# Kernel optimization log

Hardware: AMD Instinct MI355X
Metric: run time of the kernel (lower is better)

The kernel has to match this reference:

```python
import jax, jax.numpy as jnp
import numpy as np

LAMBD = 0.1  # lambd from __init__

N_POINTS = 262144
D_EMBED = 512
N_CLUSTERS = 64


def setup_inputs() -> dict:
    key = jax.random.key(0)
    k1, k2 = jax.random.split(key)
    x = jax.random.normal(k1, (N_POINTS, D_EMBED), dtype=jnp.float32)
    # original init: uniform(-1, 1)
    centroids = jax.random.uniform(k2, (N_CLUSTERS, D_EMBED), dtype=jnp.float32, minval=-1.0, maxval=1.0)
    return {"x": x, "centroids": centroids, "alpha": 100}


def reference(x, centroids, alpha):
    # stack_dist[i, n] = sum_d (x[n,d] - centroids[i,d])^2, fused via the
    x2 = jnp.sum(x * x, axis=1)                      # [N]
    c2 = jnp.sum(centroids * centroids, axis=1)      # [k]
    cross = jnp.einsum('nd,kd->kn', x, centroids)    # [k, N]
    dist = x2[None, :] + c2[:, None] - 2.0 * cross   # [k, N]
    # exp(-alpha*(dist - min)) / sum == softmax(-alpha*dist) along the k axis
    soft = jax.nn.softmax(-jnp.float32(alpha) * dist, axis=0)  # [k, N]
    k_means_loss = LAMBD * jnp.mean(jnp.sum(dist * soft, axis=0))
    return k_means_loss
```

## Files before the change

### kernel.cpp

```cpp
#include <hip/hip_runtime.h>
#include <hip/hip_bf16.h>

#define N_POINTS   262144
#define D_EMBED    512
#define N_CLUSTERS 64
#define LAMBD      0.1f

#define BLK_PTS 64
#define KC      128
#define NCHUNK  (D_EMBED / KC)
#define ROWP    (KC + 8)

typedef __attribute__((ext_vector_type(8))) short  short8;
typedef __attribute__((ext_vector_type(4))) float  f32x4;

__device__ __forceinline__ unsigned short f2bf(float f) {
    union { float f; unsigned u; } v; v.f = f;
    unsigned u = v.u;
    return (unsigned short)((u + 0x7FFFu + ((u >> 16) & 1u)) >> 16);
}

__global__ void prep_kernel(const float* __restrict__ cent,
                            float* __restrict__ c2_ws,
                            unsigned short* __restrict__ afrag_ws,
                            float* __restrict__ out) {
    const int k    = blockIdx.x;
    const int lane = threadIdx.x;
    const float* row = cent + (size_t)k * D_EMBED;

    float4 v0 = ((const float4*)row)[lane * 2 + 0];
    float4 v1 = ((const float4*)row)[lane * 2 + 1];

    float s = v0.x*v0.x + v0.y*v0.y + v0.z*v0.z + v0.w*v0.w
            + v1.x*v1.x + v1.y*v1.y + v1.z*v1.z + v1.w*v1.w;
    #pragma unroll
    for (int m = 1; m < 64; m <<= 1) s += __shfl_xor(s, m);
    if (lane == 0) c2_ws[k] = s;

    const int sstep = lane >> 2;
    const int q     = lane & 3;
    const int t     = k >> 4;
    const size_t idx8 = ((size_t)(sstep * 4 + t) * 64 + q * 16 + (k & 15)) * 8;

    ushort4 h0, h1;
    h0.x = f2bf(v0.x); h0.y = f2bf(v0.y); h0.z = f2bf(v0.z); h0.w = f2bf(v0.w);
    h1.x = f2bf(v1.x); h1.y = f2bf(v1.y); h1.z = f2bf(v1.z); h1.w = f2bf(v1.w);
    *(ushort4*)&afrag_ws[idx8 + 0] = h0;
    *(ushort4*)&afrag_ws[idx8 + 4] = h1;

    if (k == 0 && lane == 0) *out = 0.0f;
}

__global__ __launch_bounds__(256, 4)
void main_kernel(const float* __restrict__ x,
                 const int* __restrict__ alpha_p,
                 const float* __restrict__ c2_ws,
                 const unsigned short* __restrict__ afrag_ws,
                 float* __restrict__ out) {
    __shared__ unsigned short xlds[BLK_PTS * ROWP];
    __shared__ float c2s[N_CLUSTERS];
    __shared__ float x2s[BLK_PTS];
    __shared__ float blocksum_s[4];

    const int tid  = threadIdx.x;
    const int lane = tid & 63;
    const int w    = tid >> 6;
    const size_t base = (size_t)blockIdx.x * BLK_PTS;

    if (tid < 64) { c2s[tid] = c2_ws[tid]; x2s[tid] = 0.0f; }
    __syncthreads();

    const float alpha = (float)alpha_p[0];
    const int p = lane & 15;
    const int q = lane >> 4;

    f32x4 acc[4] = {f32x4{0,0,0,0}, f32x4{0,0,0,0}, f32x4{0,0,0,0}, f32x4{0,0,0,0}};

    for (int c = 0; c < NCHUNK; ++c) {
        #pragma unroll
        for (int it = 0; it < 8; ++it) {
            const int f    = it * 256 + tid;
            const int row  = f >> 5;
            const int col4 = f & 31;
            float4 v = ((const float4*)(x + (base + row) * D_EMBED + c * KC))[col4];

            float sq = v.x*v.x + v.y*v.y + v.z*v.z + v.w*v.w;
            sq += __shfl_xor(sq, 1);
            sq += __shfl_xor(sq, 2);
            sq += __shfl_xor(sq, 4);
            sq += __shfl_xor(sq, 8);
            sq += __shfl_xor(sq, 16);
            if ((lane & 31) == 0) x2s[row] += sq;

            ushort4 h;
            h.x = f2bf(v.x); h.y = f2bf(v.y); h.z = f2bf(v.z); h.w = f2bf(v.w);
            *(ushort4*)&xlds[row * ROWP + col4 * 4] = h;
        }
        __syncthreads();

        #pragma unroll
        for (int sl = 0; sl < 4; ++sl) {
            const int s = c * 4 + sl;
            short8 b = *(const short8*)&xlds[(16 * w + p) * ROWP + sl * 32 + q * 8];
            #pragma unroll
            for (int t = 0; t < 4; ++t) {
                short8 a = *(const short8*)&afrag_ws[((size_t)(s * 4 + t) * 64 + lane) * 8];
                acc[t] = __builtin_amdgcn_mfma_f32_16x16x32_bf16(a, b, acc[t], 0, 0, 0);
            }
        }
        __syncthreads();
    }

    const float x2 = x2s[16 * w + p];
    float dist[16];
    float minv = 1e30f;
    #pragma unroll
    for (int t = 0; t < 4; ++t) {
        #pragma unroll
        for (int r = 0; r < 4; ++r) {
            const int cl = 16 * t + q * 4 + r;
            const float d = x2 + c2s[cl] - 2.0f * acc[t][r];
            dist[t * 4 + r] = d;
            minv = fminf(minv, d);
        }
    }
    minv = fminf(minv, __shfl_xor(minv, 16));
    minv = fminf(minv, __shfl_xor(minv, 32));

    float esum = 0.0f, wsum = 0.0f;
    #pragma unroll
    for (int i = 0; i < 16; ++i) {
        const float e = __expf(-alpha * (dist[i] - minv));
        esum += e;
        wsum += dist[i] * e;
    }
    esum += __shfl_xor(esum, 16);
    esum += __shfl_xor(esum, 32);
    wsum += __shfl_xor(wsum, 16);
    wsum += __shfl_xor(wsum, 32);

    float pv = wsum / esum;
    #pragma unroll
    for (int m = 1; m < 64; m <<= 1) pv += __shfl_xor(pv, m);

    if (lane == 0) blocksum_s[w] = pv;
    __syncthreads();
    if (tid == 0) {
        const float T = blocksum_s[0] + blocksum_s[1] + blocksum_s[2] + blocksum_s[3];
        atomicAdd(out, T * (LAMBD / (4.0f * (float)N_POINTS)));
    }
}

extern "C" void kernel_launch(void* const* d_in, const int* in_sizes, int n_in,
                              void* d_out, int out_size, void* d_ws, size_t ws_size,
                              hipStream_t stream) {
    const float* x      = (const float*)d_in[0];
    const float* cent   = (const float*)d_in[1];
    const int*   alphap = (const int*)d_in[2];
    float* out = (float*)d_out;

    float*          c2_ws = (float*)d_ws;
    unsigned short* afrag = (unsigned short*)((char*)d_ws + 256);

    hipLaunchKernelGGL(prep_kernel, dim3(N_CLUSTERS), dim3(64), 0, stream,
                       cent, c2_ws, afrag, out);
    hipLaunchKernelGGL(main_kernel, dim3(N_POINTS / BLK_PTS), dim3(256), 0, stream,
                       x, alphap, c2_ws, afrag, out);
}
```

Measured before the change: 714.3 us.

## Load x directly into 32x32x16 MFMA operands, dropping LDS staging

Each wave now handles 32 points and loads its x rows straight from global memory into registers, converting them to bf16 operands for 32x32x16 MFMA. This removes the LDS tile, the syncthreads, and the per-row shuffle reductions of the squared norm. Each lane sums the squared norm for its own slice of the row, and one shuffle finishes it. The centroid fragments are re-laid out in the prep kernel to match the new MFMA operand shape. In exchange, the per-lane global loads are strided by row (each lane reads 32 bytes per step from a different row), which may hurt coalescing.

```diff
diff --git a/kernel.cpp b/kernel.cpp
--- a/kernel.cpp
+++ b/kernel.cpp
@@ -6,13 +6,11 @@
 #define N_CLUSTERS 64
 #define LAMBD      0.1f
 
-#define BLK_PTS 64
-#define KC      128
-#define NCHUNK  (D_EMBED / KC)
-#define ROWP    (KC + 8)
+#define PTS_PER_WAVE  32
+#define PTS_PER_BLK   128
 
-typedef __attribute__((ext_vector_type(8))) short  short8;
-typedef __attribute__((ext_vector_type(4))) float  f32x4;
+typedef __attribute__((ext_vector_type(8)))  short short8;
+typedef __attribute__((ext_vector_type(16))) float f32x16;
 
 __device__ __forceinline__ unsigned short f2bf(float f) {
     union { float f; unsigned u; } v; v.f = f;
@@ -22,7 +20,7 @@
 
 __global__ void prep_kernel(const float* __restrict__ cent,
                             float* __restrict__ c2_ws,
-                            unsigned short* __restrict__ afrag_ws,
+                            unsigned short* __restrict__ afrag,
                             float* __restrict__ out) {
     const int k    = blockIdx.x;
     const int lane = threadIdx.x;
@@ -37,16 +35,17 @@
     for (int m = 1; m < 64; m <<= 1) s += __shfl_xor(s, m);
     if (lane == 0) c2_ws[k] = s;
 
-    const int sstep = lane >> 2;
-    const int q     = lane & 3;
-    const int t     = k >> 4;
-    const size_t idx8 = ((size_t)(sstep * 4 + t) * 64 + q * 16 + (k & 15)) * 8;
+    const int st = lane >> 1;
+    const int h  = lane & 1;
+    const int t  = k >> 5;
+    const int m  = k & 31;
+    const size_t idx8 = ((size_t)(st * 2 + t) * 64 + m + 32 * h) * 8;
 
     ushort4 h0, h1;
     h0.x = f2bf(v0.x); h0.y = f2bf(v0.y); h0.z = f2bf(v0.z); h0.w = f2bf(v0.w);
     h1.x = f2bf(v1.x); h1.y = f2bf(v1.y); h1.z = f2bf(v1.z); h1.w = f2bf(v1.w);
-    *(ushort4*)&afrag_ws[idx8 + 0] = h0;
-    *(ushort4*)&afrag_ws[idx8 + 4] = h1;
+    *(ushort4*)&afrag[idx8 + 0] = h0;
+    *(ushort4*)&afrag[idx8 + 4] = h1;
 
     if (k == 0 && lane == 0) *out = 0.0f;
 }
@@ -55,99 +54,82 @@
 void main_kernel(const float* __restrict__ x,
                  const int* __restrict__ alpha_p,
                  const float* __restrict__ c2_ws,
-                 const unsigned short* __restrict__ afrag_ws,
+                 const unsigned short* __restrict__ afrag,
                  float* __restrict__ out) {
-    __shared__ unsigned short xlds[BLK_PTS * ROWP];
     __shared__ float c2s[N_CLUSTERS];
-    __shared__ float x2s[BLK_PTS];
-    __shared__ float blocksum_s[4];
+    __shared__ float bsum[4];
 
     const int tid  = threadIdx.x;
     const int lane = tid & 63;
     const int w    = tid >> 6;
-    const size_t base = (size_t)blockIdx.x * BLK_PTS;
 
-    if (tid < 64) { c2s[tid] = c2_ws[tid]; x2s[tid] = 0.0f; }
+    if (tid < 64) c2s[tid] = c2_ws[tid];
     __syncthreads();
 
     const float alpha = (float)alpha_p[0];
-    const int p = lane & 15;
-    const int q = lane >> 4;
+    const int n = lane & 31;
+    const int h = lane >> 5;
+    const size_t pt = (size_t)blockIdx.x * PTS_PER_BLK + w * PTS_PER_WAVE + n;
+    const float* xp = x + pt * D_EMBED + 8 * h;
 
-    f32x4 acc[4] = {f32x4{0,0,0,0}, f32x4{0,0,0,0}, f32x4{0,0,0,0}, f32x4{0,0,0,0}};
+    f32x16 acc0, acc1;
+    #pragma unroll
+    for (int r = 0; r < 16; ++r) { acc0[r] = 0.0f; acc1[r] = 0.0f; }
 
-    for (int c = 0; c < NCHUNK; ++c) {
-        #pragma unroll
-        for (int it = 0; it < 8; ++it) {
-            const int f    = it * 256 + tid;
-            const int row  = f >> 5;
-            const int col4 = f & 31;
-            float4 v = ((const float4*)(x + (base + row) * D_EMBED + c * KC))[col4];
+    float x2 = 0.0f;
+    #pragma unroll 4
+    for (int s = 0; s < 32; ++s) {
+        float4 u0 = *(const float4*)(xp + 16 * s);
+        float4 u1 = *(const float4*)(xp + 16 * s + 4);
 
-            float sq = v.x*v.x + v.y*v.y + v.z*v.z + v.w*v.w;
-            sq += __shfl_xor(sq, 1);
-            sq += __shfl_xor(sq, 2);
-            sq += __shfl_xor(sq, 4);
-            sq += __shfl_xor(sq, 8);
-            sq += __shfl_xor(sq, 16);
-            if ((lane & 31) == 0) x2s[row] += sq;
+        x2 += u0.x*u0.x + u0.y*u0.y + u0.z*u0.z + u0.w*u0.w
+            + u1.x*u1.x + u1.y*u1.y + u1.z*u1.z + u1.w*u1.w;
 
-            ushort4 h;
-            h.x = f2bf(v.x); h.y = f2bf(v.y); h.z = f2bf(v.z); h.w = f2bf(v.w);
-            *(ushort4*)&xlds[row * ROWP + col4 * 4] = h;
-        }
-        __syncthreads();
+        short8 b;
+        b[0] = (short)f2bf(u0.x); b[1] = (short)f2bf(u0.y);
+        b[2] = (short)f2bf(u0.z); b[3] = (short)f2bf(u0.w);
+        b[4] = (short)f2bf(u1.x); b[5] = (short)f2bf(u1.y);
+        b[6] = (short)f2bf(u1.z); b[7] = (short)f2bf(u1.w);
 
-        #pragma unroll
-        for (int sl = 0; sl < 4; ++sl) {
-            const int s = c * 4 + sl;
-            short8 b = *(const short8*)&xlds[(16 * w + p) * ROWP + sl * 32 + q * 8];
-            #pragma unroll
-            for (int t = 0; t < 4; ++t) {
-                short8 a = *(const short8*)&afrag_ws[((size_t)(s * 4 + t) * 64 + lane) * 8];
-                acc[t] = __builtin_amdgcn_mfma_f32_16x16x32_bf16(a, b, acc[t], 0, 0, 0);
-            }
-        }
-        __syncthreads();
+        short8 a0 = *(const short8*)&afrag[((size_t)(s * 2 + 0) * 64 + lane) * 8];
+        short8 a1 = *(const short8*)&afrag[((size_t)(s * 2 + 1) * 64 + lane) * 8];
+
+        acc0 = __builtin_amdgcn_mfma_f32_32x32x16_bf16(a0, b, acc0, 0, 0, 0);
+        acc1 = __builtin_amdgcn_mfma_f32_32x32x16_bf16(a1, b, acc1, 0, 0, 0);
     }
+    x2 += __shfl_xor(x2, 32);
 
-    const float x2 = x2s[16 * w + p];
-    float dist[16];
     float minv = 1e30f;
     #pragma unroll
-    for (int t = 0; t < 4; ++t) {
-        #pragma unroll
-        for (int r = 0; r < 4; ++r) {
-            const int cl = 16 * t + q * 4 + r;
-            const float d = x2 + c2s[cl] - 2.0f * acc[t][r];
-            dist[t * 4 + r] = d;
-            minv = fminf(minv, d);
-        }
+    for (int r = 0; r < 16; ++r) {
+        const int rr = (r & 3) + 8 * (r >> 2) + 4 * h;
+        const float d0 = x2 + c2s[rr]      - 2.0f * acc0[r];
+        const float d1 = x2 + c2s[rr + 32] - 2.0f * acc1[r];
+        acc0[r] = d0; acc1[r] = d1;
+        minv = fminf(minv, fminf(d0, d1));
     }
-    minv = fminf(minv, __shfl_xor(minv, 16));
     minv = fminf(minv, __shfl_xor(minv, 32));
 
     float esum = 0.0f, wsum = 0.0f;
     #pragma unroll
-    for (int i = 0; i < 16; ++i) {
-        const float e = __expf(-alpha * (dist[i] - minv));
-        esum += e;
-        wsum += dist[i] * e;
+    for (int r = 0; r < 16; ++r) {
+        const float e0 = __expf(-alpha * (acc0[r] - minv));
+        const float e1 = __expf(-alpha * (acc1[r] - minv));
+        esum += e0 + e1;
+        wsum += acc0[r] * e0 + acc1[r] * e1;
     }
-    esum += __shfl_xor(esum, 16);
     esum += __shfl_xor(esum, 32);
-    wsum += __shfl_xor(wsum, 16);
     wsum += __shfl_xor(wsum, 32);
 
     float pv = wsum / esum;
     #pragma unroll
     for (int m = 1; m < 64; m <<= 1) pv += __shfl_xor(pv, m);
 
-    if (lane == 0) blocksum_s[w] = pv;
+    if (lane == 0) bsum[w] = pv;
     __syncthreads();
     if (tid == 0) {
-        const float T = blocksum_s[0] + blocksum_s[1] + blocksum_s[2] + blocksum_s[3];
-        atomicAdd(out, T * (LAMBD / (4.0f * (float)N_POINTS)));
+        const float T = bsum[0] + bsum[1] + bsum[2] + bsum[3];
+        atomicAdd(out, T * (LAMBD / (2.0f * (float)N_POINTS)));
     }
 }
 
@@ -164,6 +146,6 @@
 
     hipLaunchKernelGGL(prep_kernel, dim3(N_CLUSTERS), dim3(64), 0, stream,
                        cent, c2_ws, afrag, out);
-    hipLaunchKernelGGL(main_kernel, dim3(N_POINTS / BLK_PTS), dim3(256), 0, stream,
+    hipLaunchKernelGGL(main_kernel, dim3(N_POINTS / PTS_PER_BLK), dim3(256), 0, stream,
                        x, alphap, c2_ws, afrag, out);
 }
```

Measured after the change: 691.8 us. -3.2%, faster.
